# Performance work log

Hardware: AMD Instinct MI355X
Metric: run time of the kernel (lower is better)

Reference implementation:

```python
import jax, jax.numpy as jnp
import numpy as np

N = 4096

def setup_inputs() -> dict:
    key = jax.random.key(0)
    k1, k2, k3 = jax.random.split(key, 3)
    x = jax.random.normal(k1, (N, N), dtype=jnp.float32)
    # nn.Linear(N, N, bias=False) weight matrices, shape [out, in] = [N, N]
    s = 1.0 / np.sqrt(N)
    W_r = jax.random.uniform(k2, (N, N), dtype=jnp.float32, minval=-s, maxval=s)
    W_i = jax.random.uniform(k3, (N, N), dtype=jnp.float32, minval=-s, maxval=s)
    return {"x": x, "W_r": W_r, "W_i": W_i}

def reference(x, W_r, W_i):
    # Row pass: fft_in_rows[i] = Linear_real(x[i]) + 1j * Linear_imag(x[i])
    #   => R = x @ W_r^T + 1j * (x @ W_i^T)
    R_r = x @ W_r.T            # [N, N]
    R_i = x @ W_i.T            # [N, N]
    # Column pass: fft_in_cols[:, i] = fft_in_rows[:, i] @ (W_r + 1j W_i)
    #   => C = W^T @ R with W = W_r + 1j W_i (complex matmul in real arithmetic)
    C_r = W_r.T @ R_r - W_i.T @ R_i
    C_i = W_r.T @ R_i + W_i.T @ R_r
    # res = cat([real, imag], dim=1) -> [N, 2N]
    return jnp.concatenate([C_r, C_i], axis=1)
```

## Files before the change

kernel.cpp:

```cpp
#include <hip/hip_runtime.h>
#include <hip/hip_bf16.h>

#define NN 4096

typedef unsigned short u16;
using bf16x8 = __attribute__((ext_vector_type(8))) short;
using f32x4  = __attribute__((ext_vector_type(4))) float;
using u32x4  = __attribute__((ext_vector_type(4))) unsigned int;

__device__ inline u16 f2bf(float f) {
    union { float f; unsigned u; } c; c.f = f;
    unsigned r = (c.u + 0x7fffu + ((c.u >> 16) & 1u)) >> 16;
    return (u16)r;
}
__device__ inline float bf2f(u16 b) {
    union { unsigned u; float f; } c; c.u = ((unsigned)b) << 16;
    return c.f;
}

__device__ inline void gld16(const void* g, void* l) {
    __builtin_amdgcn_global_load_lds(
        (const __attribute__((address_space(1))) void*)g,
        (__attribute__((address_space(3))) void*)l, 16, 0, 0);
}

__device__ inline bf16x8 negbf(bf16x8 v) {
    u32x4 u; __builtin_memcpy(&u, &v, 16);
    u ^= 0x80008000u;
    bf16x8 r; __builtin_memcpy(&r, &u, 16);
    return r;
}

__global__ __launch_bounds__(256) void cvt_bf16(const float* __restrict__ s,
                                                u16* __restrict__ d) {
    size_t i = ((size_t)blockIdx.x * 256 + threadIdx.x) * 8;
    float4 v0 = *(const float4*)(s + i);
    float4 v1 = *(const float4*)(s + i + 4);
    bf16x8 o;
    o[0] = (short)f2bf(v0.x); o[1] = (short)f2bf(v0.y);
    o[2] = (short)f2bf(v0.z); o[3] = (short)f2bf(v0.w);
    o[4] = (short)f2bf(v1.x); o[5] = (short)f2bf(v1.y);
    o[6] = (short)f2bf(v1.z); o[7] = (short)f2bf(v1.w);
    *(bf16x8*)(d + i) = o;
}

__global__ __launch_bounds__(256) void tr_cvt(const float* __restrict__ s,
                                              u16* __restrict__ d) {
    __shared__ float t[32][33];
    int x  = blockIdx.x * 32 + threadIdx.x;
    int y0 = blockIdx.y * 32;
#pragma unroll
    for (int j = 0; j < 32; j += 8)
        t[threadIdx.y + j][threadIdx.x] = s[(size_t)(y0 + threadIdx.y + j) * NN + x];
    __syncthreads();
    int x2 = blockIdx.y * 32 + threadIdx.x;
    int y2 = blockIdx.x * 32;
#pragma unroll
    for (int j = 0; j < 32; j += 8)
        d[(size_t)(y2 + threadIdx.y + j) * NN + x2] = f2bf(t[threadIdx.x][threadIdx.y + j]);
}

__global__ __launch_bounds__(256) void presum(const u16* __restrict__ a,
                                              const u16* __restrict__ b,
                                              u16* __restrict__ d) {
    size_t i = ((size_t)blockIdx.x * 256 + threadIdx.x) * 8;
    bf16x8 va = *(const bf16x8*)(a + i);
    bf16x8 vb = *(const bf16x8*)(b + i);
    bf16x8 o;
#pragma unroll
    for (int j = 0; j < 8; j++)
        o[j] = (short)f2bf(bf2f((u16)va[j]) + bf2f((u16)vb[j]));
    *(bf16x8*)(d + i) = o;
}

__global__ __launch_bounds__(256) void combine(float* __restrict__ out,
                                               const float* __restrict__ M2) {
    size_t i = ((size_t)blockIdx.x * 256 + threadIdx.x) * 4;
    size_t m = i >> 12, n = i & 4095;
    float4 v1 = *(float4*)(out + m * 8192 + n);
    float4 v3 = *(float4*)(out + m * 8192 + 4096 + n);
    float4 v2 = *(const float4*)(M2 + m * 4096 + n);
    float4 cr, ci;
    cr.x = v1.x - v2.x; ci.x = v3.x - v1.x - v2.x;
    cr.y = v1.y - v2.y; ci.y = v3.y - v1.y - v2.y;
    cr.z = v1.z - v2.z; ci.z = v3.z - v1.z - v2.z;
    cr.w = v1.w - v2.w; ci.w = v3.w - v1.w - v2.w;
    *(float4*)(out + m * 8192 + n) = cr;
    *(float4*)(out + m * 8192 + 4096 + n) = ci;
}

#define P_BAR  __builtin_amdgcn_s_barrier()
#define P_SCH  __builtin_amdgcn_sched_barrier(0)
#define P_LGKM do { asm volatile("s_waitcnt lgkmcnt(0)" ::: "memory"); \
                    __builtin_amdgcn_sched_barrier(0); } while (0)
#define VMW(N) do { asm volatile("s_waitcnt vmcnt(" #N ")" ::: "memory"); \
                    __builtin_amdgcn_sched_barrier(0); } while (0)

#define CHAIN(AF, BF, ACC) do { \
    __builtin_amdgcn_s_setprio(1); \
    _Pragma("unroll") \
    for (int i_ = 0; i_ < 4; i_++) \
        _Pragma("unroll") \
        for (int j_ = 0; j_ < 4; j_++) \
            ACC[i_][j_] = __builtin_amdgcn_mfma_f32_16x16x32_bf16(AF[i_], BF[j_], ACC[i_][j_], 0, 0, 0); \
    __builtin_amdgcn_s_setprio(0); \
} while (0)

#define RD4(DST, CC, TILE, BASE) do { \
    _Pragma("unroll") \
    for (int i_ = 0; i_ < 4; i_++) \
        DST[i_] = *(const bf16x8*)&sm[CC][TILE][((BASE) + i_ * 16 + rl) * 32 + kg]; \
} while (0)


__global__ __launch_bounds__(256, 2) void gemm_pass1(
    const u16* __restrict__ Ar, const u16* __restrict__ Ai,
    const u16* __restrict__ B,
    u16* __restrict__ Cr, u16* __restrict__ Ci) {
    __shared__ u16 sm[2][3][4096];

    const int brow = blockIdx.y * 128;
    const int bcol = blockIdx.x * 128;

    const int tid  = threadIdx.x;
    const int lane = tid & 63;
    const int wid  = tid >> 6;
    const int wm   = (wid >> 1) * 64;
    const int wn   = (wid & 1) * 64;

    f32x4 accr[4][4] = {};
    f32x4 acci[4][4] = {};

    const int r0 = tid >> 2;
    const int lb = (tid & 3) ^ ((r0 >> 1) & 3);
    const size_t aoff0 = (size_t)(brow + r0) * NN + lb * 8;
    const size_t aoff1 = aoff0 + (size_t)64 * NN;
    const size_t boff0 = (size_t)(bcol + r0) * NN + lb * 8;
    const size_t boff1 = boff0 + (size_t)64 * NN;
    const int rl = lane & 15;
    const int kg = ((lane >> 4) ^ ((rl >> 1) & 3)) * 8;

#define T0(b, kk) gld16(Ar + aoff0 + (kk), &sm[b][0][tid * 8])
#define T1(b, kk) gld16(Ar + aoff1 + (kk), &sm[b][0][2048 + tid * 8])
#define T2(b, kk) gld16(Ai + aoff0 + (kk), &sm[b][1][tid * 8])
#define T3(b, kk) gld16(Ai + aoff1 + (kk), &sm[b][1][2048 + tid * 8])
#define T4(b, kk) gld16(B  + boff0 + (kk), &sm[b][2][tid * 8])
#define T5(b, kk) gld16(B  + boff1 + (kk), &sm[b][2][2048 + tid * 8])

#define KSTEP1(CC, NB, KN, DOSTG, V0, V1) do { \
    bf16x8 af[4], ag[4], bb[4]; \
    RD4(af, CC, 0, wm); RD4(bb, CC, 2, wn); \
    if (DOSTG) { T0(NB, KN); T1(NB, KN); T4(NB, KN); T5(NB, KN); } \
    VMW(V0); P_BAR; P_LGKM; \
    CHAIN(af, bb, accr); \
    RD4(ag, CC, 1, wm); \
    P_LGKM; \
    if (DOSTG) { T2(NB, KN); T3(NB, KN); } \
    VMW(V1); P_BAR; \
    CHAIN(ag, bb, acci); \
} while (0)

    T0(0, 0); T1(0, 0); T4(0, 0); T5(0, 0); T2(0, 0); T3(0, 0);
    VMW(2); P_BAR;
    for (int t = 0; t < NN / 32 - 1; ++t) {
        const int cc = t & 1, nb = cc ^ 1;
        KSTEP1(cc, nb, (size_t)(t + 1) * 32, 1, 4, 2);
    }
    KSTEP1(1, 0, 0, 0, 0, 0);

    const int rg = (lane >> 4) * 4;
#pragma unroll
    for (int i = 0; i < 4; i++)
#pragma unroll
        for (int j = 0; j < 4; j++) {
            int col = bcol + wn + j * 16 + rl;
#pragma unroll
            for (int r = 0; r < 4; r++) {
                int row = brow + wm + i * 16 + rg + r;
                Cr[(size_t)row * NN + col] = f2bf(accr[i][j][r]);
                Ci[(size_t)row * NN + col] = f2bf(acci[i][j][r]);
            }
        }
}

#define SGA(NB, KN) do { \
    gld16(A + aoff0 + (KN), &sm2[NB][0][tid * 8]); \
    gld16(A + aoff1 + (KN), &sm2[NB][0][4096 + tid * 8]); \
} while (0)
#define SGB(NB, KN) do { \
    gld16(Bp + boff0 + (KN), &sm2[NB][1][tid * 8]); \
    gld16(Bp + boff1 + (KN), &sm2[NB][1][4096 + tid * 8]); \
} while (0)

#define K256(CB, NB, KN, DOSTG, V) do { \
    bf16x8 a[4], b[4], c[4]; \
    VMW(V); P_BAR; P_SCH; \
     \
    _Pragma("unroll") \
    for (int i_ = 0; i_ < 4; i_++) \
        a[i_] = *(const bf16x8*)&sm2[CB][0][(wr128 + i_ * 16 + rl) * 32 + kg]; \
    _Pragma("unroll") \
    for (int j_ = 0; j_ < 4; j_++) \
        b[j_] = *(const bf16x8*)&sm2[CB][1][(wc64 + j_ * 16 + rl) * 32 + kg]; \
    if (DOSTG) SGA(NB, KN); \
    P_LGKM; \
    __builtin_amdgcn_s_setprio(1); \
    _Pragma("unroll") \
    for (int i_ = 0; i_ < 4; i_++) \
        _Pragma("unroll") \
        for (int j_ = 0; j_ < 4; j_++) \
            acc[i_][j_] = __builtin_amdgcn_mfma_f32_16x16x32_bf16(a[i_], b[j_], acc[i_][j_], 0, 0, 0); \
    __builtin_amdgcn_s_setprio(0); \
     \
    _Pragma("unroll") \
    for (int i_ = 0; i_ < 4; i_++) \
        c[i_] = *(const bf16x8*)&sm2[CB][0][(wr128 + 64 + i_ * 16 + rl) * 32 + kg]; \
    if (DOSTG) SGB(NB, KN); \
    P_LGKM; \
    __builtin_amdgcn_s_setprio(1); \
    _Pragma("unroll") \
    for (int i_ = 0; i_ < 4; i_++) \
        _Pragma("unroll") \
        for (int j_ = 0; j_ < 4; j_++) \
            acc[4 + i_][j_] = __builtin_amdgcn_mfma_f32_16x16x32_bf16(c[i_], b[j_], acc[4 + i_][j_], 0, 0, 0); \
    __builtin_amdgcn_s_setprio(0); \
} while (0)

template <bool F32OUT>
__global__ __launch_bounds__(512, 2) void gemm256k(
    const u16* __restrict__ A, const u16* __restrict__ Bp,
    u16* __restrict__ Cb, float* __restrict__ Cf, int cstride) {
    __shared__ u16 sm2[4][2][8192];

    const int brow = blockIdx.y * 256;
    const int bcol = blockIdx.x * 256;

    const int tid  = threadIdx.x;
    const int lane = tid & 63;
    const int wid  = tid >> 6;
    const int wr128 = (wid >> 2) * 128;
    const int wc64  = (wid & 3) * 64;
    const int rl = lane & 15;
    const int kq = lane >> 4;
    const int kg = (kq ^ ((rl >> 1) & 3)) * 8;

    const int r0 = tid >> 2;
    const int lb = (tid & 3) ^ ((r0 >> 1) & 3);
    const size_t aoff0 = (size_t)(brow + r0) * NN + lb * 8;
    const size_t aoff1 = aoff0 + (size_t)128 * NN;
    const size_t boff0 = (size_t)(bcol + r0) * NN + lb * 8;
    const size_t boff1 = boff0 + (size_t)128 * NN;

    f32x4 acc[8][4] = {};

    SGA(0, 0); SGB(0, 0); SGA(1, 32); SGB(1, 32);

    for (int tb = 0; tb < 31; ++tb) {
        const size_t k0 = (size_t)tb * 128;
        K256(0, 2, k0 + 64,  1, 4);
        K256(1, 3, k0 + 96,  1, 4);
        K256(2, 0, k0 + 128, 1, 4);
        K256(3, 1, k0 + 160, 1, 4);
    }
    K256(0, 2, 4032, 1, 4);
    K256(1, 3, 4064, 1, 4);
    K256(2, 0, 0,    0, 4);
    K256(3, 0, 0,    0, 0);

    const int rg = kq * 4;
#pragma unroll
    for (int fr = 0; fr < 8; fr++)
#pragma unroll
        for (int fc = 0; fc < 4; fc++) {
            const int col = bcol + wc64 + fc * 16 + rl;
#pragma unroll
            for (int e = 0; e < 4; e++) {
                const int row = brow + wr128 + fr * 16 + rg + e;
                if (F32OUT)
                    Cf[(size_t)row * cstride + col] = acc[fr][fc][e];
                else
                    Cb[(size_t)row * NN + col] = f2bf(acc[fr][fc][e]);
            }
        }
}

extern "C" void kernel_launch(void* const* d_in, const int* in_sizes, int n_in,
                              void* d_out, int out_size, void* d_ws, size_t ws_size,
                              hipStream_t stream) {
    const float* x  = (const float*)d_in[0];
    const float* Wr = (const float*)d_in[1];
    const float* Wi = (const float*)d_in[2];
    float* out = (float*)d_out;

    const size_t SZ = (size_t)NN * NN;
    u16* ws = (u16*)d_ws;
    u16* s0 = ws;
    u16* s1 = ws + SZ;
    u16* s2 = ws + 2 * SZ;
    u16* s3 = ws + 3 * SZ;
    u16* s4 = ws + 4 * SZ;
    u16* s5 = ws + 5 * SZ;
    float* M2 = (float*)s2;

    cvt_bf16<<<8192, 256, 0, stream>>>(x,  s0);
    cvt_bf16<<<8192, 256, 0, stream>>>(Wr, s1);
    cvt_bf16<<<8192, 256, 0, stream>>>(Wi, s2);

    gemm_pass1<<<dim3(32, 32), 256, 0, stream>>>(s1, s2, s0, s3, s4);

    tr_cvt<<<dim3(128, 128), dim3(32, 8), 0, stream>>>(Wr, s0);
    tr_cvt<<<dim3(128, 128), dim3(32, 8), 0, stream>>>(Wi, s1);
    presum<<<8192, 256, 0, stream>>>(s0, s1, s2);
    presum<<<8192, 256, 0, stream>>>(s3, s4, s5);

    gemm256k<true><<<dim3(16, 16), 512, 0, stream>>>(s2, s5, nullptr, out + NN, 2 * NN);
    gemm256k<true><<<dim3(16, 16), 512, 0, stream>>>(s0, s3, nullptr, out,      2 * NN);
    gemm256k<true><<<dim3(16, 16), 512, 0, stream>>>(s1, s4, nullptr, M2,       NN);

    combine<<<16384, 256, 0, stream>>>(out, M2);
}
```

Measured before the change: 774.7 us.

## Fuse combine into GEMM epilogue, merge weight transposes, reuse 256-tile GEMM for pass one

Replaces the custom dual-output 128-tile first-pass GEMM with two launches of the 256-tile gemm256k kernel that write bf16 outputs. The two transpose-convert kernels and the weight presum become one wprep kernel that transposes Wr and Wi and writes their sum in a single pass. The final combine kernel is folded into the third GEMM's epilogue, which reads the existing outputs and writes the real and imaginary results directly, removing the M2 buffer. This cuts kernel launches and global memory traffic, but pass one now reads the shared B operand twice instead of once.

```diff
diff --git a/kernel.cpp b/kernel.cpp
--- a/kernel.cpp
+++ b/kernel.cpp
@@ -6,7 +6,6 @@
 typedef unsigned short u16;
 using bf16x8 = __attribute__((ext_vector_type(8))) short;
 using f32x4  = __attribute__((ext_vector_type(4))) float;
-using u32x4  = __attribute__((ext_vector_type(4))) unsigned int;
 
 __device__ inline u16 f2bf(float f) {
     union { float f; unsigned u; } c; c.f = f;
@@ -22,13 +21,6 @@
     __builtin_amdgcn_global_load_lds(
         (const __attribute__((address_space(1))) void*)g,
         (__attribute__((address_space(3))) void*)l, 16, 0, 0);
-}
-
-__device__ inline bf16x8 negbf(bf16x8 v) {
-    u32x4 u; __builtin_memcpy(&u, &v, 16);
-    u ^= 0x80008000u;
-    bf16x8 r; __builtin_memcpy(&r, &u, 16);
-    return r;
 }
 
 __global__ __launch_bounds__(256) void cvt_bf16(const float* __restrict__ s,
@@ -44,20 +36,31 @@
     *(bf16x8*)(d + i) = o;
 }
 
-__global__ __launch_bounds__(256) void tr_cvt(const float* __restrict__ s,
-                                              u16* __restrict__ d) {
-    __shared__ float t[32][33];
+__global__ __launch_bounds__(256) void wprep(const float* __restrict__ Wr,
+                                             const float* __restrict__ Wi,
+                                             u16* __restrict__ WrT,
+                                             u16* __restrict__ WiT,
+                                             u16* __restrict__ SA) {
+    __shared__ float tr[32][33], ti[32][33];
     int x  = blockIdx.x * 32 + threadIdx.x;
     int y0 = blockIdx.y * 32;
 #pragma unroll
-    for (int j = 0; j < 32; j += 8)
-        t[threadIdx.y + j][threadIdx.x] = s[(size_t)(y0 + threadIdx.y + j) * NN + x];
+    for (int j = 0; j < 32; j += 8) {
+        tr[threadIdx.y + j][threadIdx.x] = Wr[(size_t)(y0 + threadIdx.y + j) * NN + x];
+        ti[threadIdx.y + j][threadIdx.x] = Wi[(size_t)(y0 + threadIdx.y + j) * NN + x];
+    }
     __syncthreads();
     int x2 = blockIdx.y * 32 + threadIdx.x;
     int y2 = blockIdx.x * 32;
 #pragma unroll
-    for (int j = 0; j < 32; j += 8)
-        d[(size_t)(y2 + threadIdx.y + j) * NN + x2] = f2bf(t[threadIdx.x][threadIdx.y + j]);
+    for (int j = 0; j < 32; j += 8) {
+        float a = tr[threadIdx.x][threadIdx.y + j];
+        float b = ti[threadIdx.x][threadIdx.y + j];
+        size_t o = (size_t)(y2 + threadIdx.y + j) * NN + x2;
+        WrT[o] = f2bf(a);
+        WiT[o] = f2bf(b);
+        SA[o]  = f2bf(a + b);
+    }
 }
 
 __global__ __launch_bounds__(256) void presum(const u16* __restrict__ a,
@@ -73,115 +76,12 @@
     *(bf16x8*)(d + i) = o;
 }
 
-__global__ __launch_bounds__(256) void combine(float* __restrict__ out,
-                                               const float* __restrict__ M2) {
-    size_t i = ((size_t)blockIdx.x * 256 + threadIdx.x) * 4;
-    size_t m = i >> 12, n = i & 4095;
-    float4 v1 = *(float4*)(out + m * 8192 + n);
-    float4 v3 = *(float4*)(out + m * 8192 + 4096 + n);
-    float4 v2 = *(const float4*)(M2 + m * 4096 + n);
-    float4 cr, ci;
-    cr.x = v1.x - v2.x; ci.x = v3.x - v1.x - v2.x;
-    cr.y = v1.y - v2.y; ci.y = v3.y - v1.y - v2.y;
-    cr.z = v1.z - v2.z; ci.z = v3.z - v1.z - v2.z;
-    cr.w = v1.w - v2.w; ci.w = v3.w - v1.w - v2.w;
-    *(float4*)(out + m * 8192 + n) = cr;
-    *(float4*)(out + m * 8192 + 4096 + n) = ci;
-}
-
 #define P_BAR  __builtin_amdgcn_s_barrier()
 #define P_SCH  __builtin_amdgcn_sched_barrier(0)
 #define P_LGKM do { asm volatile("s_waitcnt lgkmcnt(0)" ::: "memory"); \
                     __builtin_amdgcn_sched_barrier(0); } while (0)
 #define VMW(N) do { asm volatile("s_waitcnt vmcnt(" #N ")" ::: "memory"); \
                     __builtin_amdgcn_sched_barrier(0); } while (0)
-
-#define CHAIN(AF, BF, ACC) do { \
-    __builtin_amdgcn_s_setprio(1); \
-    _Pragma("unroll") \
-    for (int i_ = 0; i_ < 4; i_++) \
-        _Pragma("unroll") \
-        for (int j_ = 0; j_ < 4; j_++) \
-            ACC[i_][j_] = __builtin_amdgcn_mfma_f32_16x16x32_bf16(AF[i_], BF[j_], ACC[i_][j_], 0, 0, 0); \
-    __builtin_amdgcn_s_setprio(0); \
-} while (0)
-
-#define RD4(DST, CC, TILE, BASE) do { \
-    _Pragma("unroll") \
-    for (int i_ = 0; i_ < 4; i_++) \
-        DST[i_] = *(const bf16x8*)&sm[CC][TILE][((BASE) + i_ * 16 + rl) * 32 + kg]; \
-} while (0)
-
-
-__global__ __launch_bounds__(256, 2) void gemm_pass1(
-    const u16* __restrict__ Ar, const u16* __restrict__ Ai,
-    const u16* __restrict__ B,
-    u16* __restrict__ Cr, u16* __restrict__ Ci) {
-    __shared__ u16 sm[2][3][4096];
-
-    const int brow = blockIdx.y * 128;
-    const int bcol = blockIdx.x * 128;
-
-    const int tid  = threadIdx.x;
-    const int lane = tid & 63;
-    const int wid  = tid >> 6;
-    const int wm   = (wid >> 1) * 64;
-    const int wn   = (wid & 1) * 64;
-
-    f32x4 accr[4][4] = {};
-    f32x4 acci[4][4] = {};
-
-    const int r0 = tid >> 2;
-    const int lb = (tid & 3) ^ ((r0 >> 1) & 3);
-    const size_t aoff0 = (size_t)(brow + r0) * NN + lb * 8;
-    const size_t aoff1 = aoff0 + (size_t)64 * NN;
-    const size_t boff0 = (size_t)(bcol + r0) * NN + lb * 8;
-    const size_t boff1 = boff0 + (size_t)64 * NN;
-    const int rl = lane & 15;
-    const int kg = ((lane >> 4) ^ ((rl >> 1) & 3)) * 8;
-
-#define T0(b, kk) gld16(Ar + aoff0 + (kk), &sm[b][0][tid * 8])
-#define T1(b, kk) gld16(Ar + aoff1 + (kk), &sm[b][0][2048 + tid * 8])
-#define T2(b, kk) gld16(Ai + aoff0 + (kk), &sm[b][1][tid * 8])
-#define T3(b, kk) gld16(Ai + aoff1 + (kk), &sm[b][1][2048 + tid * 8])
-#define T4(b, kk) gld16(B  + boff0 + (kk), &sm[b][2][tid * 8])
-#define T5(b, kk) gld16(B  + boff1 + (kk), &sm[b][2][2048 + tid * 8])
-
-#define KSTEP1(CC, NB, KN, DOSTG, V0, V1) do { \
-    bf16x8 af[4], ag[4], bb[4]; \
-    RD4(af, CC, 0, wm); RD4(bb, CC, 2, wn); \
-    if (DOSTG) { T0(NB, KN); T1(NB, KN); T4(NB, KN); T5(NB, KN); } \
-    VMW(V0); P_BAR; P_LGKM; \
-    CHAIN(af, bb, accr); \
-    RD4(ag, CC, 1, wm); \
-    P_LGKM; \
-    if (DOSTG) { T2(NB, KN); T3(NB, KN); } \
-    VMW(V1); P_BAR; \
-    CHAIN(ag, bb, acci); \
-} while (0)
-
-    T0(0, 0); T1(0, 0); T4(0, 0); T5(0, 0); T2(0, 0); T3(0, 0);
-    VMW(2); P_BAR;
-    for (int t = 0; t < NN / 32 - 1; ++t) {
-        const int cc = t & 1, nb = cc ^ 1;
-        KSTEP1(cc, nb, (size_t)(t + 1) * 32, 1, 4, 2);
-    }
-    KSTEP1(1, 0, 0, 0, 0, 0);
-
-    const int rg = (lane >> 4) * 4;
-#pragma unroll
-    for (int i = 0; i < 4; i++)
-#pragma unroll
-        for (int j = 0; j < 4; j++) {
-            int col = bcol + wn + j * 16 + rl;
-#pragma unroll
-            for (int r = 0; r < 4; r++) {
-                int row = brow + wm + i * 16 + rg + r;
-                Cr[(size_t)row * NN + col] = f2bf(accr[i][j][r]);
-                Ci[(size_t)row * NN + col] = f2bf(acci[i][j][r]);
-            }
-        }
-}
 
 #define SGA(NB, KN) do { \
     gld16(A + aoff0 + (KN), &sm2[NB][0][tid * 8]); \
@@ -195,7 +95,6 @@
 #define K256(CB, NB, KN, DOSTG, V) do { \
     bf16x8 a[4], b[4], c[4]; \
     VMW(V); P_BAR; P_SCH; \
-     \
     _Pragma("unroll") \
     for (int i_ = 0; i_ < 4; i_++) \
         a[i_] = *(const bf16x8*)&sm2[CB][0][(wr128 + i_ * 16 + rl) * 32 + kg]; \
@@ -211,7 +110,6 @@
         for (int j_ = 0; j_ < 4; j_++) \
             acc[i_][j_] = __builtin_amdgcn_mfma_f32_16x16x32_bf16(a[i_], b[j_], acc[i_][j_], 0, 0, 0); \
     __builtin_amdgcn_s_setprio(0); \
-     \
     _Pragma("unroll") \
     for (int i_ = 0; i_ < 4; i_++) \
         c[i_] = *(const bf16x8*)&sm2[CB][0][(wr128 + 64 + i_ * 16 + rl) * 32 + kg]; \
@@ -226,10 +124,10 @@
     __builtin_amdgcn_s_setprio(0); \
 } while (0)
 
-template <bool F32OUT>
+template <int OM>
 __global__ __launch_bounds__(512, 2) void gemm256k(
     const u16* __restrict__ A, const u16* __restrict__ Bp,
-    u16* __restrict__ Cb, float* __restrict__ Cf, int cstride) {
+    u16* __restrict__ Cb, float* __restrict__ Cf, int cs) {
     __shared__ u16 sm2[4][2][8192];
 
     const int brow = blockIdx.y * 256;
@@ -276,10 +174,17 @@
 #pragma unroll
             for (int e = 0; e < 4; e++) {
                 const int row = brow + wr128 + fr * 16 + rg + e;
-                if (F32OUT)
-                    Cf[(size_t)row * cstride + col] = acc[fr][fc][e];
-                else
+                if (OM == 0) {
                     Cb[(size_t)row * NN + col] = f2bf(acc[fr][fc][e]);
+                } else if (OM == 1) {
+                    Cf[(size_t)row * cs + col] = acc[fr][fc][e];
+                } else {
+                    float m2 = acc[fr][fc][e];
+                    float v1 = Cf[(size_t)row * cs + col];
+                    float v3 = Cf[(size_t)row * cs + 4096 + col];
+                    Cf[(size_t)row * cs + col]        = v1 - m2;
+                    Cf[(size_t)row * cs + 4096 + col] = v3 - v1 - m2;
+                }
             }
         }
 }
@@ -300,22 +205,18 @@
     u16* s3 = ws + 3 * SZ;
     u16* s4 = ws + 4 * SZ;
     u16* s5 = ws + 5 * SZ;
-    float* M2 = (float*)s2;
 
     cvt_bf16<<<8192, 256, 0, stream>>>(x,  s0);
     cvt_bf16<<<8192, 256, 0, stream>>>(Wr, s1);
     cvt_bf16<<<8192, 256, 0, stream>>>(Wi, s2);
 
-    gemm_pass1<<<dim3(32, 32), 256, 0, stream>>>(s1, s2, s0, s3, s4);
-
-    tr_cvt<<<dim3(128, 128), dim3(32, 8), 0, stream>>>(Wr, s0);
-    tr_cvt<<<dim3(128, 128), dim3(32, 8), 0, stream>>>(Wi, s1);
-    presum<<<8192, 256, 0, stream>>>(s0, s1, s2);
+    gemm256k<0><<<dim3(16, 16), 512, 0, stream>>>(s1, s0, s3, nullptr, 0);
+    gemm256k<0><<<dim3(16, 16), 512, 0, stream>>>(s2, s0, s4, nullptr, 0);
+
+    wprep<<<dim3(128, 128), dim3(32, 8), 0, stream>>>(Wr, Wi, s0, s1, s2);
     presum<<<8192, 256, 0, stream>>>(s3, s4, s5);
 
-    gemm256k<true><<<dim3(16, 16), 512, 0, stream>>>(s2, s5, nullptr, out + NN, 2 * NN);
-    gemm256k<true><<<dim3(16, 16), 512, 0, stream>>>(s0, s3, nullptr, out,      2 * NN);
-    gemm256k<true><<<dim3(16, 16), 512, 0, stream>>>(s1, s4, nullptr, M2,       NN);
-
-    combine<<<16384, 256, 0, stream>>>(out, M2);
-}
+    gemm256k<1><<<dim3(16, 16), 512, 0, stream>>>(s2, s5, nullptr, out + NN, 2 * NN);
+    gemm256k<1><<<dim3(16, 16), 512, 0, stream>>>(s0, s3, nullptr, out,      2 * NN);
+    gemm256k<2><<<dim3(16, 16), 512, 0, stream>>>(s1, s4, nullptr, out,      2 * NN);
+}
```

Result: no change. 774.5 us (-0.0%).
